# Optimization experiments

Measured on AMD Instinct MI355X. Metric: run time of the kernel, lower is better.

Reference implementation:

```python
import jax, jax.numpy as jnp
import numpy as np

B, S, D = 1, 2048, 4096          # batch, seqlen, model dim
H, KVH, HD = 32, 8, 128          # query heads, kv heads, head dim
W = 1024                         # sliding window
ROPE_THETA = 10000.0


def _rope(t, cos, sin):
    # t: [b, s, h, hd]; complex pairing matches torch.view_as_complex on reshape(..., hd//2, 2)
    a = t[..., 0::2]
    b = t[..., 1::2]
    out_r = a * cos - b * sin
    out_i = a * sin + b * cos
    return jnp.stack([out_r, out_i], axis=-1).reshape(t.shape)


def setup_inputs() -> dict:
    key = jax.random.key(0)
    ks = jax.random.split(key, 5)
    x = jax.random.normal(ks[0], (1, B, S, D), dtype=jnp.float32)
    wq = jax.random.normal(ks[1], (H * HD, D), dtype=jnp.float32) * 0.02
    wk = jax.random.normal(ks[2], (KVH * HD, D), dtype=jnp.float32) * 0.02
    wv = jax.random.normal(ks[3], (KVH * HD, D), dtype=jnp.float32) * 0.02
    wo = jax.random.normal(ks[4], (D, H * HD), dtype=jnp.float32) * 0.02
    # rotary frequencies: freqs_cis[s, hd/2] = exp(i * s * theta^{-2k/hd})
    inv_freq = 1.0 / (ROPE_THETA ** (jnp.arange(0, HD, 2, dtype=jnp.float32) / HD))
    angles = jnp.arange(S, dtype=jnp.float32)[:, None] * inv_freq[None, :]  # [S, HD/2]
    freqs_cos = jnp.cos(angles)
    freqs_sin = jnp.sin(angles)
    # sliding-window causal mask (additive)
    i = jnp.arange(S)
    allowed = (i[:, None] >= i[None, :]) & (i[:, None] - i[None, :] < W)
    mask = jnp.where(allowed, 0.0, -1e9).astype(jnp.float32)
    positions = jnp.arange(S, dtype=jnp.int64)
    return {"x": x, "wq": wq, "wk": wk, "wv": wv, "wo": wo,
            "freqs_cos": freqs_cos, "freqs_sin": freqs_sin,
            "mask": mask, "positions": positions}


def reference(x, wq, wk, wv, wo, freqs_cos, freqs_sin, mask, positions):
    xs = x[0]                                   # [B, S, D]
    xq = (xs @ wq.T).reshape(B, S, H, HD)
    xk = (xs @ wk.T).reshape(B, S, KVH, HD)
    xv = (xs @ wv.T).reshape(B, S, KVH, HD)
    cos = freqs_cos[None, :, None, :]           # [1, S, 1, HD/2]
    sin = freqs_sin[None, :, None, :]
    xq = _rope(xq, cos, sin)
    xk = _rope(xk, cos, sin)
    # GQA: repeat_interleave kv heads to match query heads (prefill path)
    rep = H // KVH
    k = jnp.repeat(xk, rep, axis=2)             # [B, S, H, HD]
    v = jnp.repeat(xv, rep, axis=2)
    scale = HD ** -0.5
    scores = jnp.einsum('bqhd,bkhd->bhqk', xq, k) * scale + mask[None, None]
    probs = jax.nn.softmax(scores, axis=-1)
    out = jnp.einsum('bhqk,bkhd->bqhd', probs, v).reshape(B, S, H * HD)
    return (out @ wo.T)[None]                   # [1, B, S, D]
```

## Files before the change

### kernel.cpp

```cpp
#include <hip/hip_runtime.h>
#include <hip/hip_bf16.h>


typedef __attribute__((ext_vector_type(8))) short short8;
typedef __attribute__((ext_vector_type(4))) float floatx4;
typedef unsigned short u16;
typedef unsigned int u32;

__device__ __forceinline__ u16 f2bf(float f) {
  u32 u = __builtin_bit_cast(u32, f);
  u32 r = u + 0x7FFFu + ((u >> 16) & 1u);
  return (u16)(r >> 16);
}

#define GLDS16(g, l)                                                     \
  __builtin_amdgcn_global_load_lds(                                      \
      (const __attribute__((address_space(1))) u32*)(g),                 \
      (__attribute__((address_space(3))) u32*)(l), 16, 0, 0)

__global__ __launch_bounds__(256) void cast_in(
    const float* __restrict__ x, const float* __restrict__ wq,
    const float* __restrict__ wk, const float* __restrict__ wv,
    u16* __restrict__ xb, u16* __restrict__ wqb, u16* __restrict__ wkb,
    u16* __restrict__ wvb) {
  const int tid = blockIdx.x * blockDim.x + threadIdx.x;
  const int stride = gridDim.x * blockDim.x;
  auto seg = [&](const float* __restrict__ in, u16* __restrict__ out, int n4) {
    for (int i = tid; i < n4; i += stride) {
      float4 v = ((const float4*)in)[i];
      ushort4 o;
      o.x = f2bf(v.x); o.y = f2bf(v.y); o.z = f2bf(v.z); o.w = f2bf(v.w);
      ((ushort4*)out)[i] = o;
    }
  };
  seg(x, xb, 2097152);
  seg(wq, wqb, 4194304);
  seg(wk, wkb, 1048576);
  seg(wv, wvb, 1048576);
}

__global__ __launch_bounds__(512, 2) void gemm_qkv(
    const u16* __restrict__ A, const u16* __restrict__ B, u16* __restrict__ Cq,
    u16* __restrict__ Ck, u16* __restrict__ Cv, const float* __restrict__ fcos,
    const float* __restrict__ fsin) {
  constexpr int BM = 256, BN = 192;
  constexpr int WR = 64, WC = 96;
  constexpr int MFR = 4, NFR = 6;
  constexpr int ASZ = BM * 128;
  constexpr int BSZ = BN * 128;
  constexpr int NCA = 4, NCB = 3;
  __shared__ u16 lds[(2 * ASZ + 3 * BSZ) / 2];
  const int K = 4096;

  const int bm = blockIdx.x & 7;
  const int bx = blockIdx.x >> 3;
  const int m0 = bm * BM, n0 = bx * BN;

  const int t = threadIdx.x, l = t & 63, w = t >> 6;
  const int li = l & 15, g = l >> 4;
  const int wm = w >> 1, wn = w & 1;

  const int srow = t >> 3;
  const int sslot = (t & 7) ^ (srow & 7);
  const u16* gA = A + (size_t)(m0 + srow) * K + sslot * 8;
  const u16* gB = B + (size_t)(n0 + srow) * K + sslot * 8;
  const int dst = t * 16;

  char* A0p = (char*)lds;
  char* A1p = A0p + ASZ;
  char* B0p = A0p + 2 * ASZ;
  char* B1p = B0p + BSZ;
  char* B2p = B1p + BSZ;

  auto stA = [&](char* base, int kt, int c) {
    GLDS16(gA + (size_t)c * 64 * K + kt, base + c * 8192 + dst);
  };
  auto stB = [&](char* base, int kt, int c) {
    GLDS16(gB + (size_t)c * 64 * K + kt, base + c * 8192 + dst);
  };

  int offA[2][MFR], offB[2][NFR];
#pragma unroll
  for (int kh = 0; kh < 2; kh++) {
#pragma unroll
    for (int mf = 0; mf < MFR; mf++) {
      int r = wm * WR + mf * 16 + li;
      offA[kh][mf] = r * 128 + ((((kh << 2) | g) ^ (r & 7)) << 4);
    }
#pragma unroll
    for (int nf = 0; nf < NFR; nf++) {
      int r = wn * WC + nf * 16 + li;
      offB[kh][nf] = r * 128 + ((((kh << 2) | g) ^ (r & 7)) << 4);
    }
  }

  floatx4 acc[MFR][NFR] = {};
  const int NT = K / 64;

#pragma unroll
  for (int c = 0; c < NCB; c++) stB(B0p, 0, c);
#pragma unroll
  for (int c = 0; c < NCA; c++) stA(A0p, 0, c);
#pragma unroll
  for (int c = 0; c < NCB; c++) stB(B1p, 64, c);
  asm volatile("s_waitcnt vmcnt(3)" ::: "memory");
  __builtin_amdgcn_s_barrier();

  for (int tt = 0; tt < NT; ++tt) {
    const char* Ac = A0p;
    const char* Bc = B0p;
    const int kt1 = (tt + 1) * 64, kt2 = (tt + 2) * 64;
    const bool s1 = (tt + 1 < NT), s2 = (tt + 2 < NT);

    short8 a0[MFR], b0[NFR], a1[MFR], b1[NFR];
#pragma unroll
    for (int nf = 0; nf < NFR; nf++) b0[nf] = *(const short8*)(Bc + offB[0][nf]);
#pragma unroll
    for (int mf = 0; mf < MFR; mf++) a0[mf] = *(const short8*)(Ac + offA[0][mf]);
    if (s1) {
#pragma unroll
      for (int c = 0; c < NCA; c++) stA(A1p, kt1, c);
    }
#pragma unroll
    for (int mf = 0; mf < MFR; mf++)
#pragma unroll
      for (int nf = 0; nf < NFR; nf++)
        acc[mf][nf] = __builtin_amdgcn_mfma_f32_16x16x32_bf16(a0[mf], b0[nf], acc[mf][nf], 0, 0, 0);
#pragma unroll
    for (int nf = 0; nf < NFR; nf++) b1[nf] = *(const short8*)(Bc + offB[1][nf]);
#pragma unroll
    for (int mf = 0; mf < MFR; mf++) a1[mf] = *(const short8*)(Ac + offA[1][mf]);
    if (s2) {
#pragma unroll
      for (int c = 0; c < NCB; c++) stB(B2p, kt2, c);
    }
#pragma unroll
    for (int mf = 0; mf < MFR; mf++)
#pragma unroll
      for (int nf = 0; nf < NFR; nf++)
        acc[mf][nf] = __builtin_amdgcn_mfma_f32_16x16x32_bf16(a1[mf], b1[nf], acc[mf][nf], 0, 0, 0);
    if (s2)      asm volatile("s_waitcnt vmcnt(3)" ::: "memory");
    else if (s1) asm volatile("s_waitcnt vmcnt(0)" ::: "memory");
    __builtin_amdgcn_s_barrier();

    char* tmpA = A0p; A0p = A1p; A1p = tmpA;
    char* tmpB = B0p; B0p = B1p; B1p = B2p; B2p = tmpB;
  }

  const float scale = 0.08838834764831845f;
#pragma unroll
  for (int mf = 0; mf < MFR; mf++) {
#pragma unroll
    for (int nf = 0; nf < NFR; nf++) {
      const int row0 = m0 + wm * WR + mf * 16 + 4 * g;
      const int c = n0 + wn * WC + nf * 16 + li;
      if (c < 5120) {
        const int hd = c & 127;
        const int pp = hd >> 1;
        const bool even = (hd & 1) == 0;
#pragma unroll
        for (int r = 0; r < 4; r++) {
          const int row = row0 + r;
          float cv = fcos[row * 64 + pp];
          float sv = fsin[row * 64 + pp];
          float v = acc[mf][nf][r];
          float pv = __shfl_xor(v, 1);
          float o = even ? (v * cv - pv * sv) : (pv * sv + v * cv);
          if (c < 4096) {
            Cq[(size_t)row * 4096 + c] = f2bf(o * scale);
          } else {
            Ck[(size_t)row * 1024 + (c - 4096)] = f2bf(o);
          }
        }
      } else {
        u32 lo = (u32)f2bf(acc[mf][nf][0]) | ((u32)f2bf(acc[mf][nf][1]) << 16);
        u32 hi = (u32)f2bf(acc[mf][nf][2]) | ((u32)f2bf(acc[mf][nf][3]) << 16);
        uint2 val; val.x = lo; val.y = hi;
        *(uint2*)(&Cv[(size_t)(c - 5120) * 2048 + row0]) = val;
      }
    }
  }
}

__global__ __launch_bounds__(256, 2) void gemm_o(
    const u16* __restrict__ A, const u16* __restrict__ B, float* __restrict__ C) {
  constexpr int ASZ = 128 * 128;
  constexpr int BSZ = 128 * 128;
  __shared__ u16 lds[(2 * ASZ + 3 * BSZ) / 2];
  const int K = 4096;

  const int xcd = blockIdx.x & 7;
  const int j = blockIdx.x >> 3;
  const int bm = xcd * 2 + (j & 1);
  const int bx = j >> 1;
  const int m0 = bm * 128, n0 = bx * 128;

  const int t = threadIdx.x, l = t & 63, w = t >> 6;
  const int li = l & 15, g = l >> 4;
  const int wm = w >> 1, wn = w & 1;

  const int srow = t >> 3;
  const int sslot = (t & 7) ^ (srow & 7);
  const u16* gA = A + (size_t)(m0 + srow) * K + sslot * 8;
  const u16* gB = B + (size_t)(n0 + srow) * K + sslot * 8;
  const int dst = t * 16;

  char* A0p = (char*)lds;
  char* A1p = A0p + ASZ;
  char* B0p = A0p + 2 * ASZ;
  char* B1p = B0p + BSZ;
  char* B2p = B1p + BSZ;

  auto stA = [&](char* base, int kt, int c) {
    GLDS16(gA + (size_t)c * 32 * K + kt, base + c * 4096 + dst);
  };
  auto stB = [&](char* base, int kt, int c) {
    GLDS16(gB + (size_t)c * 32 * K + kt, base + c * 4096 + dst);
  };

  int offA[2][4], offB[2][4];
#pragma unroll
  for (int kh = 0; kh < 2; kh++) {
#pragma unroll
    for (int mf = 0; mf < 4; mf++) {
      int r = wm * 64 + mf * 16 + li;
      offA[kh][mf] = r * 128 + ((((kh << 2) | g) ^ (r & 7)) << 4);
    }
#pragma unroll
    for (int nf = 0; nf < 4; nf++) {
      int r = wn * 64 + nf * 16 + li;
      offB[kh][nf] = r * 128 + ((((kh << 2) | g) ^ (r & 7)) << 4);
    }
  }

  floatx4 acc[4][4] = {};
  const int NT = K / 64;

#pragma unroll
  for (int c = 0; c < 4; c++) stB(B0p, 0, c);
#pragma unroll
  for (int c = 0; c < 4; c++) stA(A0p, 0, c);
#pragma unroll
  for (int c = 0; c < 4; c++) stB(B1p, 64, c);
  asm volatile("s_waitcnt vmcnt(4)" ::: "memory");
  __builtin_amdgcn_s_barrier();

  for (int tt = 0; tt < NT; ++tt) {
    const char* Ac = A0p;
    const char* Bc = B0p;
    const int kt1 = (tt + 1) * 64, kt2 = (tt + 2) * 64;
    const bool s1 = (tt + 1 < NT), s2 = (tt + 2 < NT);

    short8 a0[4], b0[4], a1[4], b1[4];
#pragma unroll
    for (int mf = 0; mf < 4; mf++) a0[mf] = *(const short8*)(Ac + offA[0][mf]);
#pragma unroll
    for (int nf = 0; nf < 4; nf++) b0[nf] = *(const short8*)(Bc + offB[0][nf]);
    if (s1) {
#pragma unroll
      for (int c = 0; c < 4; c++) stA(A1p, kt1, c);
    }
#pragma unroll
    for (int mf = 0; mf < 4; mf++)
#pragma unroll
      for (int nf = 0; nf < 4; nf++)
        acc[mf][nf] = __builtin_amdgcn_mfma_f32_16x16x32_bf16(a0[mf], b0[nf], acc[mf][nf], 0, 0, 0);
#pragma unroll
    for (int mf = 0; mf < 4; mf++) a1[mf] = *(const short8*)(Ac + offA[1][mf]);
#pragma unroll
    for (int nf = 0; nf < 4; nf++) b1[nf] = *(const short8*)(Bc + offB[1][nf]);
    if (s2) {
#pragma unroll
      for (int c = 0; c < 4; c++) stB(B2p, kt2, c);
    }
#pragma unroll
    for (int mf = 0; mf < 4; mf++)
#pragma unroll
      for (int nf = 0; nf < 4; nf++)
        acc[mf][nf] = __builtin_amdgcn_mfma_f32_16x16x32_bf16(a1[mf], b1[nf], acc[mf][nf], 0, 0, 0);
    if (s2)      asm volatile("s_waitcnt vmcnt(4)" ::: "memory");
    else if (s1) asm volatile("s_waitcnt vmcnt(0)" ::: "memory");
    __builtin_amdgcn_s_barrier();

    char* tmpA = A0p; A0p = A1p; A1p = tmpA;
    char* tmpB = B0p; B0p = B1p; B1p = B2p; B2p = tmpB;
  }

#pragma unroll
  for (int mf = 0; mf < 4; mf++) {
#pragma unroll
    for (int nf = 0; nf < 4; nf++) {
      const int row0 = m0 + wm * 64 + mf * 16 + 4 * g;
      const int c = n0 + wn * 64 + nf * 16 + li;
#pragma unroll
      for (int r = 0; r < 4; r++) C[(size_t)(row0 + r) * 4096 + c] = acc[mf][nf][r];
    }
  }
}

__global__ __launch_bounds__(512, 2) void attn_kernel(const u16* __restrict__ Q,
                                                      const u16* __restrict__ K,
                                                      const u16* __restrict__ Vt,
                                                      u16* __restrict__ O,
                                                      const float* __restrict__ wo,
                                                      u16* __restrict__ wob) {
  __shared__ u16 Ks[64 * 128];
  __shared__ u16 Vs[128 * 64];
  __shared__ u16 Ps[8][16 * 68];

  {
    const int gid = (blockIdx.y * gridDim.x + blockIdx.x) * 512 + threadIdx.x;
#pragma unroll 4
    for (int i = 0; i < 16; i++) {
      const size_t idx = (size_t)gid + (size_t)i * 262144;
      float4 v = ((const float4*)wo)[idx];
      ushort4 o;
      o.x = f2bf(v.x); o.y = f2bf(v.y); o.z = f2bf(v.z); o.w = f2bf(v.w);
      ((ushort4*)wob)[idx] = o;
    }
  }

  const int t = threadIdx.x, l = t & 63, w = t >> 6;
  const int li = l & 15, g = l >> 4;
  const int q0 = blockIdx.x * 128;
  const int h = blockIdx.y;
  const int kvh = h >> 2;
  const int qw = q0 + w * 16;

  short8 qf[4];
  {
    const u16* qp = Q + (size_t)(qw + li) * 4096 + h * 128 + g * 8;
#pragma unroll
    for (int kk = 0; kk < 4; kk++) qf[kk] = *(const short8*)(qp + kk * 32);
  }

  const u16* gK[2];
  const u16* gV[2];
  int ldsOff[2];
#pragma unroll
  for (int i = 0; i < 2; i++) {
    int rK = (2 * w + i) * 4 + (l >> 4);
    int sK = (l & 15) ^ (rK & 7);
    gK[i] = K + (size_t)rK * 1024 + kvh * 128 + sK * 8;
    int rV = (2 * w + i) * 8 + (l >> 3);
    int sV = (l & 7) ^ (rV & 7);
    gV[i] = Vt + (size_t)(kvh * 128 + rV) * 2048 + sV * 8;
    ldsOff[i] = (2 * w + i) * 1024;
  }

  int offK[4][4];
#pragma unroll
  for (int n = 0; n < 4; n++) {
    int r = 16 * n + li;
#pragma unroll
    for (int kk = 0; kk < 4; kk++)
      offK[n][kk] = r * 256 + (((kk * 4 + g) ^ (r & 7)) << 4);
  }
  int offV[2][8];
#pragma unroll
  for (int kb = 0; kb < 2; kb++)
#pragma unroll
    for (int dt = 0; dt < 8; dt++) {
      int d = dt * 16 + li;
      offV[kb][dt] = d * 128 + (((kb * 4 + g) ^ (d & 7)) << 4);
    }

  float mrow[4] = {-1e30f, -1e30f, -1e30f, -1e30f};
  float lsum[4] = {0.f, 0.f, 0.f, 0.f};
  floatx4 accO[8] = {};

  int klo = q0 - 1023;
  if (klo < 0) klo = 0;
  klo &= ~63;
  const int nt = (q0 + 128 - klo) >> 6;

  for (int it = 0; it < nt; it++) {
    const int k0 = klo + (it << 6);
#pragma unroll
    for (int i = 0; i < 2; i++) GLDS16(gK[i] + (size_t)k0 * 1024, (char*)Ks + ldsOff[i]);
#pragma unroll
    for (int i = 0; i < 2; i++) GLDS16(gV[i] + k0, (char*)Vs + ldsOff[i]);
    asm volatile("s_waitcnt vmcnt(0)" ::: "memory");
    __builtin_amdgcn_s_barrier();

    if (k0 <= qw + 15 && k0 + 63 >= qw - 1023) {
      const char* kb = (const char*)Ks;
      const char* vb = (const char*)Vs;
      floatx4 s[4] = {};
      __builtin_amdgcn_s_setprio(1);
#pragma unroll
      for (int kk = 0; kk < 4; kk++)
#pragma unroll
        for (int n = 0; n < 4; n++) {
          short8 kf = *(const short8*)(kb + offK[n][kk]);
          s[n] = __builtin_amdgcn_mfma_f32_16x16x32_bf16(qf[kk], kf, s[n], 0, 0, 0);
        }
      __builtin_amdgcn_s_setprio(0);
      const bool full = (k0 + 63 <= qw) && (k0 >= qw + 15 - 1023);
      if (!full) {
#pragma unroll
        for (int n = 0; n < 4; n++) {
          const int kc = k0 + n * 16 + li;
#pragma unroll
          for (int r = 0; r < 4; r++) {
            const int qr = qw + 4 * g + r;
            if (kc > qr || qr - kc > 1023) s[n][r] = -__builtin_inff();
          }
        }
      }
      float rm[4];
#pragma unroll
      for (int r = 0; r < 4; r++)
        rm[r] = fmaxf(fmaxf(s[0][r], s[1][r]), fmaxf(s[2][r], s[3][r]));
#pragma unroll
      for (int msk = 1; msk <= 8; msk <<= 1)
#pragma unroll
        for (int r = 0; r < 4; r++) rm[r] = fmaxf(rm[r], __shfl_xor(rm[r], msk));
      float al[4];
#pragma unroll
      for (int r = 0; r < 4; r++) {
        float mn = fmaxf(mrow[r], rm[r]);
        al[r] = __expf(mrow[r] - mn);
        mrow[r] = mn;
        lsum[r] *= al[r];
      }
#pragma unroll
      for (int dt = 0; dt < 8; dt++)
#pragma unroll
        for (int r = 0; r < 4; r++) accO[dt][r] *= al[r];
      float rs[4] = {0.f, 0.f, 0.f, 0.f};
      u16* pw = &Ps[w][0];
#pragma unroll
      for (int n = 0; n < 4; n++)
#pragma unroll
        for (int r = 0; r < 4; r++) {
          float p = __expf(s[n][r] - mrow[r]);
          rs[r] += p;
          pw[(4 * g + r) * 68 + n * 16 + li] = f2bf(p);
        }
#pragma unroll
      for (int msk = 1; msk <= 8; msk <<= 1)
#pragma unroll
        for (int r = 0; r < 4; r++) rs[r] += __shfl_xor(rs[r], msk);
#pragma unroll
      for (int r = 0; r < 4; r++) lsum[r] += rs[r];
      short8 pa[2];
#pragma unroll
      for (int kbi = 0; kbi < 2; kbi++)
        pa[kbi] = *(const short8*)((const char*)&Ps[w][0] + li * 136 + kbi * 64 + g * 16);
      __builtin_amdgcn_s_setprio(1);
#pragma unroll
      for (int kbi = 0; kbi < 2; kbi++)
#pragma unroll
        for (int dt = 0; dt < 8; dt++) {
          short8 vf = *(const short8*)(vb + offV[kbi][dt]);
          accO[dt] = __builtin_amdgcn_mfma_f32_16x16x32_bf16(pa[kbi], vf, accO[dt], 0, 0, 0);
        }
      __builtin_amdgcn_s_setprio(0);
    }
    __builtin_amdgcn_s_barrier();
  }

  float inv[4];
#pragma unroll
  for (int r = 0; r < 4; r++) inv[r] = 1.0f / lsum[r];
#pragma unroll
  for (int dt = 0; dt < 8; dt++)
#pragma unroll
    for (int r = 0; r < 4; r++)
      O[(size_t)(qw + 4 * g + r) * 4096 + h * 128 + dt * 16 + li] =
          f2bf(accO[dt][r] * inv[r]);
}

extern "C" void kernel_launch(void* const* d_in, const int* in_sizes, int n_in,
                              void* d_out, int out_size, void* d_ws, size_t ws_size,
                              hipStream_t stream) {
  const float* x    = (const float*)d_in[0];
  const float* wq   = (const float*)d_in[1];
  const float* wk   = (const float*)d_in[2];
  const float* wv   = (const float*)d_in[3];
  const float* wo   = (const float*)d_in[4];
  const float* fcos = (const float*)d_in[5];
  const float* fsin = (const float*)d_in[6];

  u16* ws  = (u16*)d_ws;
  u16* xb  = ws;
  u16* wqb = xb + 8388608;
  u16* wkb = wqb + 16777216;
  u16* wvb = wkb + 4194304;
  u16* wob = wvb + 4194304;
  u16* Qb  = wob + 16777216;
  u16* Kb  = Qb + 8388608;
  u16* Vtb = Kb + 2097152;
  u16* AOb = Vtb + 2097152;

  cast_in<<<1536, 256, 0, stream>>>(x, wq, wk, wv, xb, wqb, wkb, wvb);
  gemm_qkv<<<256, 512, 0, stream>>>(xb, wqb, Qb, Kb, Vtb, fcos, fsin);
  attn_kernel<<<dim3(16, 32), 512, 0, stream>>>(Qb, Kb, Vtb, AOb, wo, wob);
  gemm_o<<<512, 256, 0, stream>>>(AOb, wob, (float*)d_out);
}
```

Baseline: 285.9 us.

## Restructure QKV GEMM into 256x256 tiles with eight-phase interleaved staging pipeline

```diff
diff --git a/kernel.cpp b/kernel.cpp
--- a/kernel.cpp
+++ b/kernel.cpp
@@ -39,121 +39,110 @@
   seg(wv, wvb, 1048576);
 }
 
+#define PH(tile, q, dostage, op, sT, sh, WVN) do {                            \
+    const char* ab_ = (const char*)lds + ((tile) & 1) * 32768 + wm * 16384;   \
+    const char* bb_ = (const char*)lds + 65536 + ((tile) & 1) * 32768 +       \
+                      (wn >> 1) * 16384;                                       \
+    if ((q) == 0) {                                                            \
+      _Pragma("unroll") for (int kk = 0; kk < 2; kk++)                         \
+        _Pragma("unroll") for (int nf = 0; nf < 4; nf++)                       \
+          bfr[kk][nf] = *(const short8*)(bb_ + offB[kk][nf]);                  \
+    }                                                                          \
+    short8 afr[2][2];                                                          \
+    _Pragma("unroll") for (int kk = 0; kk < 2; kk++)                           \
+      _Pragma("unroll") for (int i = 0; i < 2; i++)                            \
+        afr[i][kk] = *(const short8*)(ab_ + offA[kk][2 * (q) + i]);            \
+    if (dostage) stage(op, sT, sh);                                            \
+    __builtin_amdgcn_s_barrier();                                              \
+    asm volatile("s_waitcnt lgkmcnt(0)" ::: "memory");                         \
+    __builtin_amdgcn_s_setprio(1);                                             \
+    _Pragma("unroll") for (int i = 0; i < 2; i++)                              \
+      _Pragma("unroll") for (int nf = 0; nf < 4; nf++)                         \
+        _Pragma("unroll") for (int kk = 0; kk < 2; kk++)                       \
+          acc[2 * (q) + i][nf] = __builtin_amdgcn_mfma_f32_16x16x32_bf16(      \
+              afr[i][kk], bfr[kk][nf], acc[2 * (q) + i][nf], 0, 0, 0);         \
+    __builtin_amdgcn_s_setprio(0);                                             \
+    if ((WVN) == 0)      asm volatile("s_waitcnt vmcnt(0)" ::: "memory");      \
+    else if ((WVN) == 4) asm volatile("s_waitcnt vmcnt(4)" ::: "memory");      \
+    __builtin_amdgcn_s_barrier();                                              \
+  } while (0)
+
 __global__ __launch_bounds__(512, 2) void gemm_qkv(
     const u16* __restrict__ A, const u16* __restrict__ B, u16* __restrict__ Cq,
     u16* __restrict__ Ck, u16* __restrict__ Cv, const float* __restrict__ fcos,
     const float* __restrict__ fsin) {
-  constexpr int BM = 256, BN = 192;
-  constexpr int WR = 64, WC = 96;
-  constexpr int MFR = 4, NFR = 6;
-  constexpr int ASZ = BM * 128;
-  constexpr int BSZ = BN * 128;
-  constexpr int NCA = 4, NCB = 3;
-  __shared__ u16 lds[(2 * ASZ + 3 * BSZ) / 2];
+  __shared__ u16 lds[65536];
   const int K = 4096;
 
   const int bm = blockIdx.x & 7;
   const int bx = blockIdx.x >> 3;
-  const int m0 = bm * BM, n0 = bx * BN;
+  const int m0 = bm * 256, n0 = bx * 256;
 
   const int t = threadIdx.x, l = t & 63, w = t >> 6;
   const int li = l & 15, g = l >> 4;
-  const int wm = w >> 1, wn = w & 1;
+  const int wm = w >> 2, wn = w & 3;
 
   const int srow = t >> 3;
-  const int sslot = (t & 7) ^ (srow & 7);
-  const u16* gA = A + (size_t)(m0 + srow) * K + sslot * 8;
-  const u16* gB = B + (size_t)(n0 + srow) * K + sslot * 8;
+  const int swz = (t & 7) ^ (srow & 7);
+  const u16* gAr = A + (size_t)(m0 + srow) * K + swz * 8;
+  const u16* gBr = B + (size_t)(n0 + srow) * K + swz * 8;
   const int dst = t * 16;
 
-  char* A0p = (char*)lds;
-  char* A1p = A0p + ASZ;
-  char* B0p = A0p + 2 * ASZ;
-  char* B1p = B0p + BSZ;
-  char* B2p = B1p + BSZ;
-
-  auto stA = [&](char* base, int kt, int c) {
-    GLDS16(gA + (size_t)c * 64 * K + kt, base + c * 8192 + dst);
+  auto stage = [&](int op, int T, int h) {
+    const u16* gsrc = op ? gBr : gAr;
+    char* base = (char*)lds + op * 65536 + ((T & 1) * 2 + h) * 16384;
+#pragma unroll
+    for (int c = 0; c < 2; c++)
+      GLDS16(gsrc + (size_t)(h * 128 + c * 64) * K + T * 64,
+             base + c * 8192 + dst);
   };
-  auto stB = [&](char* base, int kt, int c) {
-    GLDS16(gB + (size_t)c * 64 * K + kt, base + c * 8192 + dst);
-  };
-
-  int offA[2][MFR], offB[2][NFR];
-#pragma unroll
-  for (int kh = 0; kh < 2; kh++) {
-#pragma unroll
-    for (int mf = 0; mf < MFR; mf++) {
-      int r = wm * WR + mf * 16 + li;
-      offA[kh][mf] = r * 128 + ((((kh << 2) | g) ^ (r & 7)) << 4);
-    }
-#pragma unroll
-    for (int nf = 0; nf < NFR; nf++) {
-      int r = wn * WC + nf * 16 + li;
-      offB[kh][nf] = r * 128 + ((((kh << 2) | g) ^ (r & 7)) << 4);
-    }
-  }
-
-  floatx4 acc[MFR][NFR] = {};
-  const int NT = K / 64;
-
-#pragma unroll
-  for (int c = 0; c < NCB; c++) stB(B0p, 0, c);
-#pragma unroll
-  for (int c = 0; c < NCA; c++) stA(A0p, 0, c);
-#pragma unroll
-  for (int c = 0; c < NCB; c++) stB(B1p, 64, c);
-  asm volatile("s_waitcnt vmcnt(3)" ::: "memory");
+
+  int offA[2][8], offB[2][4];
+#pragma unroll
+  for (int kk = 0; kk < 2; kk++) {
+#pragma unroll
+    for (int mf = 0; mf < 8; mf++) {
+      int r = mf * 16 + li;
+      offA[kk][mf] = r * 128 + ((((kk << 2) | g) ^ (r & 7)) << 4);
+    }
+#pragma unroll
+    for (int nf = 0; nf < 4; nf++) {
+      int r = (wn & 1) * 64 + nf * 16 + li;
+      offB[kk][nf] = r * 128 + ((((kk << 2) | g) ^ (r & 7)) << 4);
+    }
+  }
+
+  floatx4 acc[8][4] = {};
+  short8 bfr[2][4];
+
+  stage(0, 0, 0); stage(0, 0, 1);
+  stage(1, 0, 0); stage(1, 0, 1);
+  stage(1, 1, 0); stage(1, 1, 1);
+  asm volatile("s_waitcnt vmcnt(0)" ::: "memory");
   __builtin_amdgcn_s_barrier();
 
-  for (int tt = 0; tt < NT; ++tt) {
-    const char* Ac = A0p;
-    const char* Bc = B0p;
-    const int kt1 = (tt + 1) * 64, kt2 = (tt + 2) * 64;
-    const bool s1 = (tt + 1 < NT), s2 = (tt + 2 < NT);
-
-    short8 a0[MFR], b0[NFR], a1[MFR], b1[NFR];
-#pragma unroll
-    for (int nf = 0; nf < NFR; nf++) b0[nf] = *(const short8*)(Bc + offB[0][nf]);
-#pragma unroll
-    for (int mf = 0; mf < MFR; mf++) a0[mf] = *(const short8*)(Ac + offA[0][mf]);
-    if (s1) {
-#pragma unroll
-      for (int c = 0; c < NCA; c++) stA(A1p, kt1, c);
-    }
-#pragma unroll
-    for (int mf = 0; mf < MFR; mf++)
-#pragma unroll
-      for (int nf = 0; nf < NFR; nf++)
-        acc[mf][nf] = __builtin_amdgcn_mfma_f32_16x16x32_bf16(a0[mf], b0[nf], acc[mf][nf], 0, 0, 0);
-#pragma unroll
-    for (int nf = 0; nf < NFR; nf++) b1[nf] = *(const short8*)(Bc + offB[1][nf]);
-#pragma unroll
-    for (int mf = 0; mf < MFR; mf++) a1[mf] = *(const short8*)(Ac + offA[1][mf]);
-    if (s2) {
-#pragma unroll
-      for (int c = 0; c < NCB; c++) stB(B2p, kt2, c);
-    }
-#pragma unroll
-    for (int mf = 0; mf < MFR; mf++)
-#pragma unroll
-      for (int nf = 0; nf < NFR; nf++)
-        acc[mf][nf] = __builtin_amdgcn_mfma_f32_16x16x32_bf16(a1[mf], b1[nf], acc[mf][nf], 0, 0, 0);
-    if (s2)      asm volatile("s_waitcnt vmcnt(3)" ::: "memory");
-    else if (s1) asm volatile("s_waitcnt vmcnt(0)" ::: "memory");
-    __builtin_amdgcn_s_barrier();
-
-    char* tmpA = A0p; A0p = A1p; A1p = tmpA;
-    char* tmpB = B0p; B0p = B1p; B1p = B2p; B2p = tmpB;
+#pragma unroll 1
+  for (int J = 0; J < 32; ++J) {
+    const int a = 2 * J, b = 2 * J + 1;
+    const bool s2 = (J < 31);
+    const int w4 = s2 ? 4 : 0;
+    PH(a, 0, true, 0, b, 0, -1);
+    PH(a, 1, true, 0, b, 1, -1);
+    PH(a, 2, s2, 1, a + 2, 0, -1);
+    PH(a, 3, s2, 1, a + 2, 1, w4);
+    PH(b, 0, s2, 0, a + 2, 0, -1);
+    PH(b, 1, s2, 0, a + 2, 1, -1);
+    PH(b, 2, s2, 1, b + 2, 0, -1);
+    PH(b, 3, s2, 1, b + 2, 1, w4);
   }
 
   const float scale = 0.08838834764831845f;
 #pragma unroll
-  for (int mf = 0; mf < MFR; mf++) {
-#pragma unroll
-    for (int nf = 0; nf < NFR; nf++) {
-      const int row0 = m0 + wm * WR + mf * 16 + 4 * g;
-      const int c = n0 + wn * WC + nf * 16 + li;
+  for (int mf = 0; mf < 8; mf++) {
+#pragma unroll
+    for (int nf = 0; nf < 4; nf++) {
+      const int row0 = m0 + wm * 128 + mf * 16 + 4 * g;
+      const int c = n0 + wn * 64 + nf * 16 + li;
       if (c < 5120) {
         const int hd = c & 127;
         const int pp = hd >> 1;
@@ -495,7 +484,7 @@
   u16* AOb = Vtb + 2097152;
 
   cast_in<<<1536, 256, 0, stream>>>(x, wq, wk, wv, xb, wqb, wkb, wvb);
-  gemm_qkv<<<256, 512, 0, stream>>>(xb, wqb, Qb, Kb, Vtb, fcos, fsin);
+  gemm_qkv<<<192, 512, 0, stream>>>(xb, wqb, Qb, Kb, Vtb, fcos, fsin);
   attn_kernel<<<dim3(16, 32), 512, 0, stream>>>(Qb, Kb, Vtb, AOb, wo, wob);
   gemm_o<<<512, 256, 0, stream>>>(AOb, wob, (float*)d_out);
 }
```

Measured after the change: 309.8 us. +8.4%, slower.
